# Performance work log

Hardware: AMD Instinct MI355X
Metric: run time of the kernel (lower is better)

## Reference

```python
import jax, jax.numpy as jnp
import numpy as np

N = 50000
EPS = 1e-16


def _gat_conv(x, w, att_src, att_dst, bias, src, dst, heads, out_ch, concat):
    # x: [N, F_in]; w: [heads*out_ch, F_in]; att_*: [heads, out_ch]; bias: [heads*out_ch] or [out_ch]
    n = x.shape[0]
    xw = (x @ w.T).reshape(n, heads, out_ch)              # [N, H, C]
    a_src = jnp.einsum('nhc,hc->nh', xw, att_src)          # [N, H]
    a_dst = jnp.einsum('nhc,hc->nh', xw, att_dst)
    alpha = a_src[src] + a_dst[dst]                        # [E, H]
    alpha = jax.nn.leaky_relu(alpha, negative_slope=0.2)
    # segment softmax over destination node (every node has a self loop)
    m = jax.ops.segment_max(alpha, dst, num_segments=n)    # [N, H]
    e = jnp.exp(alpha - m[dst])
    s = jax.ops.segment_sum(e, dst, num_segments=n)        # [N, H]
    coef = e / (s[dst] + EPS)                              # [E, H]
    out = jax.ops.segment_sum(xw[src] * coef[:, :, None], dst, num_segments=n)  # [N, H, C]
    if concat:
        out = out.reshape(n, heads * out_ch)
    else:
        out = out.mean(axis=1)
    return out + bias


def setup_inputs() -> dict:
    key = jax.random.key(0)
    ks = jax.random.split(key, 8)
    F_in, H, C1, NC = 128, 2, 64, 16
    E = 1_600_000
    x = jax.random.normal(ks[0], (N, F_in), dtype=jnp.float32)
    edge_index = jax.random.randint(ks[1], (2, E), 0, N, dtype=jnp.int64)
    w1 = jax.random.normal(ks[2], (H * C1, F_in), dtype=jnp.float32) / np.sqrt(F_in)
    att_src1 = jax.random.normal(ks[3], (H, C1), dtype=jnp.float32) / np.sqrt(C1)
    att_dst1 = jax.random.normal(ks[4], (H, C1), dtype=jnp.float32) / np.sqrt(C1)
    b1 = jnp.zeros((H * C1,), dtype=jnp.float32)
    w2 = jax.random.normal(ks[5], (NC, H * C1), dtype=jnp.float32) / np.sqrt(H * C1)
    att_src2 = jax.random.normal(ks[6], (1, NC), dtype=jnp.float32) / np.sqrt(NC)
    att_dst2 = jax.random.normal(ks[7], (1, NC), dtype=jnp.float32) / np.sqrt(NC)
    b2 = jnp.zeros((NC,), dtype=jnp.float32)
    return {"x": x, "edge_index": edge_index, "w1": w1, "att_src1": att_src1,
            "att_dst1": att_dst1, "b1": b1, "w2": w2, "att_src2": att_src2,
            "att_dst2": att_dst2, "b2": b2}


def reference(x, edge_index, w1, att_src1, att_dst1, b1, w2, att_src2, att_dst2, b2):
    n = x.shape[0]
    loop = jnp.arange(n, dtype=edge_index.dtype)
    src = jnp.concatenate([edge_index[0], loop])  # PyG adds self loops by default
    dst = jnp.concatenate([edge_index[1], loop])
    h = _gat_conv(x, w1, att_src1, att_dst1, b1, src, dst, heads=2, out_ch=64, concat=True)
    h = jax.nn.relu(h)
    # dropout p=0.5 is identity in eval mode
    out = _gat_conv(h, w2, att_src2, att_dst2, b2, src, dst, heads=1, out_ch=16, concat=True)
    return out
```

## Files before the change

### kernel.cpp

```cpp
#include <hip/hip_runtime.h>
#include <hip/hip_fp16.h>


#define BSHIFT 7
#define MAXB 512
#define CAPMAX 6144
#define XS 136

using f16x8 = __attribute__((ext_vector_type(8))) _Float16;
using f16x4 = __attribute__((ext_vector_type(4))) _Float16;
using f32x4 = __attribute__((ext_vector_type(4))) float;

__device__ __forceinline__ float lrelu(float a) { return fmaxf(a, 0.2f * a); }


__global__ __launch_bounds__(256) void part_gemm1_kernel(
    const int* __restrict__ src, const int* __restrict__ dst,
    int* __restrict__ bincur, unsigned* __restrict__ binned,
    int E, int B, int CH, int CAP, int NB,
    const float* __restrict__ x, const float* __restrict__ w1,
    const float* __restrict__ as1, const float* __restrict__ ad1,
    __half* __restrict__ xw1h, float* __restrict__ asrc1,
    float* __restrict__ adst1, int N) {
  __shared__ __align__(16) char smem[(64 + 128) * XS * 2];
  int t = threadIdx.x;

  if (blockIdx.x < (unsigned)NB) {
    int* s_h = (int*)smem;
    int* s_base = s_h + MAXB;
    int* s_cur = s_base + MAXB;
    unsigned* s_pack = (unsigned*)(s_cur + MAXB);
    for (int i = t; i < B; i += 256) s_h[i] = 0;
    __syncthreads();
    int lo = blockIdx.x * CH;
    int cnt = min(CH, E - lo);
    for (int i = t; i < cnt; i += 256) {
      int d = dst[lo + i];
      int s = src[lo + i];
      atomicAdd(&s_h[d >> BSHIFT], 1);
      s_pack[i] = (unsigned)s | ((unsigned)(d & 127) << 16) |
                  ((unsigned)(d >> BSHIFT) << 23);
    }
    __syncthreads();
    for (int i = t; i < B; i += 256) {
      int c = s_h[i];
      s_base[i] = c ? (i * CAP + atomicAdd(&bincur[i], c)) : 0;
      s_cur[i] = 0;
    }
    __syncthreads();
    for (int i = t; i < cnt; i += 256) {
      unsigned e = s_pack[i];
      int b = e >> 23;
      int r = atomicAdd(&s_cur[b], 1);
      binned[s_base[b] + r] = e & 0x7FFFFFu;
    }
    return;
  }

  _Float16* lx = (_Float16*)smem;
  _Float16* lw = lx + 64 * XS;
  int n0 = (blockIdx.x - NB) * 64;

#pragma unroll
  for (int j = 0; j < 8; ++j) {
    int idx = t + 256 * j;
    int nd = idx >> 5, i4 = (idx & 31) * 4;
    int gn = n0 + nd;
    float4 v = (gn < N) ? *(const float4*)&x[(size_t)gn * 128 + i4]
                        : make_float4(0.f, 0.f, 0.f, 0.f);
    f16x4 h;
    h[0] = (_Float16)v.x; h[1] = (_Float16)v.y;
    h[2] = (_Float16)v.z; h[3] = (_Float16)v.w;
    *(f16x4*)&lx[nd * XS + i4] = h;
  }
#pragma unroll
  for (int j = 0; j < 16; ++j) {
    int idx = t + 256 * j;
    int o = idx >> 5, i4 = (idx & 31) * 4;
    float4 v = *(const float4*)&w1[(size_t)o * 128 + i4];
    f16x4 h;
    h[0] = (_Float16)v.x; h[1] = (_Float16)v.y;
    h[2] = (_Float16)v.z; h[3] = (_Float16)v.w;
    *(f16x4*)&lw[o * XS + i4] = h;
  }
  __syncthreads();

  int lane = t & 63, wv = t >> 6;
  int m16 = lane & 15, q = lane >> 4;

  f32x4 acc[8];
#pragma unroll
  for (int i = 0; i < 8; ++i) acc[i] = (f32x4){0.f, 0.f, 0.f, 0.f};

#pragma unroll
  for (int c = 0; c < 4; ++c) {
    f16x8 a = *(const f16x8*)&lx[(16 * wv + m16) * XS + c * 32 + q * 8];
#pragma unroll
    for (int tt = 0; tt < 8; ++tt) {
      f16x8 b = *(const f16x8*)&lw[(tt * 16 + m16) * XS + c * 32 + q * 8];
      acc[tt] = __builtin_amdgcn_mfma_f32_16x16x32_f16(a, b, acc[tt], 0, 0, 0);
    }
  }

#pragma unroll
  for (int tt = 0; tt < 8; ++tt) {
#pragma unroll
    for (int r = 0; r < 4; ++r) {
      lx[(16 * wv + 4 * q + r) * XS + tt * 16 + m16] = (_Float16)acc[tt][r];
    }
  }

  {
    float ps = 0.f, pd = 0.f;
    int p = q;
#pragma unroll
    for (int k = 0; k < 4; ++k) {
      f16x8 hv = *(const f16x8*)&lx[(16 * wv + m16) * XS + p * 32 + k * 8];
      float4 s0 = *(const float4*)&as1[p * 32 + k * 8];
      float4 s1 = *(const float4*)&as1[p * 32 + k * 8 + 4];
      float4 d0 = *(const float4*)&ad1[p * 32 + k * 8];
      float4 d1 = *(const float4*)&ad1[p * 32 + k * 8 + 4];
      ps += (float)hv[0] * s0.x + (float)hv[1] * s0.y + (float)hv[2] * s0.z +
            (float)hv[3] * s0.w + (float)hv[4] * s1.x + (float)hv[5] * s1.y +
            (float)hv[6] * s1.z + (float)hv[7] * s1.w;
      pd += (float)hv[0] * d0.x + (float)hv[1] * d0.y + (float)hv[2] * d0.z +
            (float)hv[3] * d0.w + (float)hv[4] * d1.x + (float)hv[5] * d1.y +
            (float)hv[6] * d1.z + (float)hv[7] * d1.w;
    }
    ps += __shfl_xor(ps, 16);
    pd += __shfl_xor(pd, 16);
    int n = n0 + 16 * wv + m16;
    if (n < N && (q == 0 || q == 2)) {
      int hh = q >> 1;
      asrc1[2 * n + hh] = ps;
      adst1[2 * n + hh] = pd;
    }
  }

#pragma unroll
  for (int i = 0; i < 4; ++i) {
    int m = q + 4 * i;
    int n = n0 + 16 * wv + m;
    if (n < N) {
      uint4 v = *(const uint4*)&lx[(16 * wv + m) * XS + m16 * 8];
      *(uint4*)&xw1h[(size_t)n * 128 + m16 * 8] = v;
    }
  }
}


__global__ __launch_bounds__(256) void bucket_build_kernel(const unsigned* __restrict__ binned,
                                                           const int* __restrict__ bincur,
                                                           int2* __restrict__ nodeseg,
                                                           unsigned short* __restrict__ csr,
                                                           int N, int CAP) {
  __shared__ int s_deg[128];
  __shared__ int s_cur[128];
  __shared__ int s_wsum;
  __shared__ unsigned s_edges[CAPMAX];
  int b = blockIdx.x;
  int lo = b * CAP, hi = lo + bincur[b];
  int cnt = hi - lo;
  int t = threadIdx.x;
  if (t < 128) s_deg[t] = 0;
  int stg = min(cnt, CAPMAX);
  for (int i = t; i < stg; i += 256) s_edges[i] = binned[lo + i];
  __syncthreads();
  for (int i = t; i < cnt; i += 256) {
    unsigned e = (i < CAPMAX) ? s_edges[i] : binned[lo + i];
    atomicAdd(&s_deg[e >> 16], 1);
  }
  __syncthreads();
  int lane = t & 63, wv = t >> 6;
  int v = (t < 128) ? s_deg[t] : 0;
  int incl = v;
#pragma unroll
  for (int off = 1; off < 64; off <<= 1) {
    int u = __shfl_up(incl, off);
    if (lane >= off) incl += u;
  }
  if (t == 63) s_wsum = incl;
  __syncthreads();
  int excl = incl - v + ((wv == 1) ? s_wsum : 0);
  if (t < 128) {
    int node = (b << BSHIFT) + t;
    if (node < N) nodeseg[node] = make_int2(lo + excl, lo + excl + v);
    s_cur[t] = lo + excl;
  }
  __syncthreads();
  for (int i = t; i < cnt; i += 256) {
    unsigned e = (i < CAPMAX) ? s_edges[i] : binned[lo + i];
    int p = atomicAdd(&s_cur[e >> 16], 1);
    csr[p] = (unsigned short)(e & 0xFFFFu);
  }
}


__global__ __launch_bounds__(256) void agg1_kernel(const __half* __restrict__ xw1h,
                                                   const float* __restrict__ asrc1,
                                                   const float* __restrict__ adst1,
                                                   const float* __restrict__ b1,
                                                   const float* __restrict__ w2,
                                                   const float* __restrict__ as2,
                                                   const float* __restrict__ ad2,
                                                   const unsigned short* __restrict__ csr,
                                                   const int2* __restrict__ nodeseg,
                                                   __half* __restrict__ xw2h,
                                                   float* __restrict__ asrc2,
                                                   float* __restrict__ adst2, int N) {
  __shared__ int s_off[4][64];
  __shared__ float2 s_w[4][64];
  int lane = threadIdx.x & 63, wv = threadIdx.x >> 6;
  int d = blockIdx.x * 4 + wv;
  if (d >= N) return;
  int c8 = lane & 15;
  int row = lane >> 4;
  int head = c8 >> 3;
  int2 seg = nodeseg[d];
  int e0 = seg.x, e1 = seg.y;
  float2 asv = *(const float2*)&asrc1[2 * d];
  float2 adv = *(const float2*)&adst1[2 * d];
  float wself = __expf(lrelu(head ? (asv.y + adv.y) : (asv.x + adv.x)));

  const char* xb = (const char*)xw1h + 16 * c8;

  float a[8];
  float sum = 0.f;
#pragma unroll
  for (int k = 0; k < 8; ++k) a[k] = 0.f;
  if (row == 0) {
    uint4 r = *(const uint4*)(xb + ((size_t)d << 8));
    const __half2* hp = (const __half2*)&r;
#pragma unroll
    for (int k = 0; k < 4; ++k) {
      float2 v = __half22float2(hp[k]);
      a[2 * k] = wself * v.x;
      a[2 * k + 1] = wself * v.y;
    }
    sum = wself;
  }

  for (int base = e0; base < e1; base += 64) {
    int cnt = min(64, e1 - base);
    if (lane < cnt) {
      int s = (int)csr[base + lane];
      float2 aa = *(const float2*)&asrc1[2 * s];
      s_off[wv][lane] = s << 8;
      float2 w;
      w.x = __expf(lrelu(aa.x + adv.x));
      w.y = __expf(lrelu(aa.y + adv.y));
      s_w[wv][lane] = w;
    }
    int j = 0;
    for (; j + 7 < cnt; j += 8) {
      int oA = s_off[wv][j + row];
      int oB = s_off[wv][j + 4 + row];
      float wA = ((const float*)&s_w[wv][j + row])[head];
      float wB = ((const float*)&s_w[wv][j + 4 + row])[head];
      uint4 rA = *(const uint4*)(xb + oA);
      uint4 rB = *(const uint4*)(xb + oB);
      const __half2* hA = (const __half2*)&rA;
      const __half2* hB = (const __half2*)&rB;
#pragma unroll
      for (int k = 0; k < 4; ++k) {
        float2 vA = __half22float2(hA[k]);
        float2 vB = __half22float2(hB[k]);
        a[2 * k] += wA * vA.x + wB * vB.x;
        a[2 * k + 1] += wA * vA.y + wB * vB.y;
      }
      sum += wA + wB;
    }
    for (; j < cnt; j += 4) {
      if (row < cnt - j) {
        int oA = s_off[wv][j + row];
        float wA = ((const float*)&s_w[wv][j + row])[head];
        uint4 rA = *(const uint4*)(xb + oA);
        const __half2* hA = (const __half2*)&rA;
#pragma unroll
        for (int k = 0; k < 4; ++k) {
          float2 vA = __half22float2(hA[k]);
          a[2 * k] += wA * vA.x;
          a[2 * k + 1] += wA * vA.y;
        }
        sum += wA;
      }
    }
  }

#pragma unroll
  for (int k = 0; k < 8; ++k) {
    a[k] += __shfl_xor(a[k], 16);
    a[k] += __shfl_xor(a[k], 32);
  }
  sum += __shfl_xor(sum, 16);
  sum += __shfl_xor(sum, 32);

  float inv = 1.f / (sum + 1e-16f);
  float4 blo = *(const float4*)&b1[8 * c8];
  float4 bhi = *(const float4*)&b1[8 * c8 + 4];
  float h[8];
  h[0] = fmaxf(a[0] * inv + blo.x, 0.f);
  h[1] = fmaxf(a[1] * inv + blo.y, 0.f);
  h[2] = fmaxf(a[2] * inv + blo.z, 0.f);
  h[3] = fmaxf(a[3] * inv + blo.w, 0.f);
  h[4] = fmaxf(a[4] * inv + bhi.x, 0.f);
  h[5] = fmaxf(a[5] * inv + bhi.y, 0.f);
  h[6] = fmaxf(a[6] * inv + bhi.z, 0.f);
  h[7] = fmaxf(a[7] * inv + bhi.w, 0.f);

  float p[4];
#pragma unroll
  for (int cc = 0; cc < 4; ++cc) {
    const float4 wlo = *(const float4*)&w2[(row * 4 + cc) * 128 + 8 * c8];
    const float4 whi = *(const float4*)&w2[(row * 4 + cc) * 128 + 8 * c8 + 4];
    p[cc] = h[0] * wlo.x + h[1] * wlo.y + h[2] * wlo.z + h[3] * wlo.w +
            h[4] * whi.x + h[5] * whi.y + h[6] * whi.z + h[7] * whi.w;
#pragma unroll
    for (int k = 1; k < 16; k <<= 1) p[cc] += __shfl_xor(p[cc], k);
  }
  float qs = 0.f, qd = 0.f;
#pragma unroll
  for (int cc = 0; cc < 4; ++cc) {
    qs += p[cc] * as2[row * 4 + cc];
    qd += p[cc] * ad2[row * 4 + cc];
  }
  qs += __shfl_xor(qs, 16);
  qs += __shfl_xor(qs, 32);
  qd += __shfl_xor(qd, 16);
  qd += __shfl_xor(qd, 32);
  if (lane == 0) {
    asrc2[d] = qs;
    adst2[d] = qd;
  }
  if (c8 == 0) {
    union {
      __half hh[4];
      uint2 u;
    } pk;
#pragma unroll
    for (int cc = 0; cc < 4; ++cc) pk.hh[cc] = __float2half(p[cc]);
    *(uint2*)&xw2h[(size_t)d * 16 + row * 4] = pk.u;
  }
}


__global__ __launch_bounds__(256) void agg2_kernel(const __half* __restrict__ xw2h,
                                                   const float* __restrict__ asrc2,
                                                   const float* __restrict__ adst2,
                                                   const float* __restrict__ b2,
                                                   const unsigned short* __restrict__ csr,
                                                   const int2* __restrict__ nodeseg,
                                                   float* __restrict__ out, int N) {
  __shared__ int s_off[4][64];
  __shared__ float s_w[4][64];
  int lane = threadIdx.x & 63, wv = threadIdx.x >> 6;
  int d = blockIdx.x * 4 + wv;
  if (d >= N) return;
  int c2 = lane & 7;
  int row = lane >> 3;
  int2 seg = nodeseg[d];
  int e0 = seg.x, e1 = seg.y;
  float advd = adst2[d];
  float wself = __expf(lrelu(asrc2[d] + advd));
  const char* xb = (const char*)xw2h + 4 * c2;

  float a0 = 0.f, a1 = 0.f, sum = 0.f;
  if (row == 0) {
    float2 v = __half22float2(*(const __half2*)(xb + (size_t)d * 32));
    a0 = wself * v.x;
    a1 = wself * v.y;
    sum = wself;
  }
  for (int base = e0; base < e1; base += 64) {
    int cnt = min(64, e1 - base);
    if (lane < cnt) {
      int s = (int)csr[base + lane];
      s_off[wv][lane] = s << 5;
      s_w[wv][lane] = __expf(lrelu(asrc2[s] + advd));
    }
    int j = 0;
    for (; j + 15 < cnt; j += 16) {
      int o0 = s_off[wv][j + row];
      int o1 = s_off[wv][j + 8 + row];
      float w0 = s_w[wv][j + row];
      float w1 = s_w[wv][j + 8 + row];
      float2 v0 = __half22float2(*(const __half2*)(xb + o0));
      float2 v1 = __half22float2(*(const __half2*)(xb + o1));
      a0 += w0 * v0.x + w1 * v1.x;
      a1 += w0 * v0.y + w1 * v1.y;
      sum += w0 + w1;
    }
    for (; j + 7 < cnt; j += 8) {
      int o0 = s_off[wv][j + row];
      float w0 = s_w[wv][j + row];
      float2 v0 = __half22float2(*(const __half2*)(xb + o0));
      a0 += w0 * v0.x;
      a1 += w0 * v0.y;
      sum += w0;
    }
    if (row < cnt - j) {
      int o0 = s_off[wv][j + row];
      float w0 = s_w[wv][j + row];
      float2 v0 = __half22float2(*(const __half2*)(xb + o0));
      a0 += w0 * v0.x;
      a1 += w0 * v0.y;
      sum += w0;
    }
  }
#pragma unroll
  for (int k = 8; k < 64; k <<= 1) {
    a0 += __shfl_xor(a0, k);
    a1 += __shfl_xor(a1, k);
    sum += __shfl_xor(sum, k);
  }
  if (lane < 8) {
    float inv = 1.f / (sum + 1e-16f);
    float2 r;
    r.x = a0 * inv + b2[2 * c2];
    r.y = a1 * inv + b2[2 * c2 + 1];
    *(float2*)&out[(size_t)d * 16 + 2 * c2] = r;
  }
}


extern "C" void kernel_launch(void* const* d_in, const int* in_sizes, int n_in,
                              void* d_out, int out_size, void* d_ws, size_t ws_size,
                              hipStream_t stream) {
  const float* x = (const float*)d_in[0];
  const int* ei = (const int*)d_in[1];
  const float* w1 = (const float*)d_in[2];
  const float* as1 = (const float*)d_in[3];
  const float* ad1 = (const float*)d_in[4];
  const float* b1 = (const float*)d_in[5];
  const float* w2 = (const float*)d_in[6];
  const float* as2 = (const float*)d_in[7];
  const float* ad2 = (const float*)d_in[8];
  const float* b2 = (const float*)d_in[9];
  float* out = (float*)d_out;

  int N = in_sizes[0] / 128;
  int E = in_sizes[1] / 2;
  const int* srcp = ei;
  const int* dstp = ei + E;

  int B = (N + (1 << BSHIFT) - 1) >> BSHIFT;
  int mean = (E + B - 1) / B;
  int CAP = (mean + mean / 4 + 512 + 255) & ~255;
  const int NB = 256;
  int CH = (E + NB - 1) / NB;
  int GB = (N + 63) / 64;

  char* p = (char*)d_ws;
  auto alloc = [&](size_t bytes) -> void* {
    void* r = (void*)p;
    p += (bytes + 255) & ~(size_t)255;
    return r;
  };
  __half* xw1h = (__half*)alloc((size_t)N * 128 * 2);
  float* asrc1 = (float*)alloc((size_t)N * 2 * 4);
  float* adst1 = (float*)alloc((size_t)N * 2 * 4);
  __half* xw2h = (__half*)alloc((size_t)N * 16 * 2);
  float* asrc2 = (float*)alloc((size_t)N * 4);
  float* adst2 = (float*)alloc((size_t)N * 4);
  int2* nodeseg = (int2*)alloc((size_t)N * 8);
  unsigned short* csr = (unsigned short*)alloc((size_t)B * CAP * 2);
  unsigned* binned = (unsigned*)alloc((size_t)B * CAP * 4);
  int* bincur = (int*)alloc((size_t)B * 4);

  hipMemsetAsync(bincur, 0, (size_t)B * 4, stream);
  part_gemm1_kernel<<<NB + GB, 256, 0, stream>>>(srcp, dstp, bincur, binned,
                                                 E, B, CH, CAP, NB,
                                                 x, w1, as1, ad1, xw1h, asrc1, adst1, N);
  bucket_build_kernel<<<B, 256, 0, stream>>>(binned, bincur, nodeseg, csr, N, CAP);
  agg1_kernel<<<(N + 3) / 4, 256, 0, stream>>>(xw1h, asrc1, adst1, b1, w2, as2, ad2,
                                               csr, nodeseg, xw2h, asrc2, adst2, N);
  agg2_kernel<<<(N + 3) / 4, 256, 0, stream>>>(xw2h, asrc2, adst2, b2, csr, nodeseg, out, N);
}
```

Before: 210.2 us.

## Split layer-1 aggregation per head and add a combine kernel for layer-2 projection

The layer-1 aggregation kernel now runs one wavefront per (node, head) instead of per node. Each head's 64 channels are covered by 8 lanes, and 8 edges are processed per step, unrolled to 16. Each head writes its partial layer-2 projection to a new fp32 buffer. A new combine kernel sums the two head partials, writes the fp16 xw2 and computes the layer-2 attention logits. The aim is more parallelism and more edges in flight per gather step, at the cost of reading the CSR and edge weights twice, extra global traffic for the partial buffer, and one more kernel launch.

```diff
diff --git a/kernel.cpp b/kernel.cpp
--- a/kernel.cpp
+++ b/kernel.cpp
@@ -196,33 +196,28 @@
 }
 
 
-__global__ __launch_bounds__(256) void agg1_kernel(const __half* __restrict__ xw1h,
-                                                   const float* __restrict__ asrc1,
-                                                   const float* __restrict__ adst1,
-                                                   const float* __restrict__ b1,
-                                                   const float* __restrict__ w2,
-                                                   const float* __restrict__ as2,
-                                                   const float* __restrict__ ad2,
-                                                   const unsigned short* __restrict__ csr,
-                                                   const int2* __restrict__ nodeseg,
-                                                   __half* __restrict__ xw2h,
-                                                   float* __restrict__ asrc2,
-                                                   float* __restrict__ adst2, int N) {
+__global__ __launch_bounds__(256) void agg1h_kernel(const __half* __restrict__ xw1h,
+                                                    const float* __restrict__ asrc1,
+                                                    const float* __restrict__ adst1,
+                                                    const float* __restrict__ b1,
+                                                    const float* __restrict__ w2,
+                                                    const unsigned short* __restrict__ csr,
+                                                    const int2* __restrict__ nodeseg,
+                                                    float* __restrict__ p_out, int N) {
   __shared__ int s_off[4][64];
-  __shared__ float2 s_w[4][64];
+  __shared__ float s_w[4][64];
   int lane = threadIdx.x & 63, wv = threadIdx.x >> 6;
-  int d = blockIdx.x * 4 + wv;
+  int head = blockIdx.x & 1;
+  int d = (blockIdx.x >> 1) * 4 + wv;
   if (d >= N) return;
-  int c8 = lane & 15;
-  int row = lane >> 4;
-  int head = c8 >> 3;
+  int c8 = lane & 7;
+  int row = lane >> 3;
   int2 seg = nodeseg[d];
   int e0 = seg.x, e1 = seg.y;
-  float2 asv = *(const float2*)&asrc1[2 * d];
-  float2 adv = *(const float2*)&adst1[2 * d];
-  float wself = __expf(lrelu(head ? (asv.y + adv.y) : (asv.x + adv.x)));
-
-  const char* xb = (const char*)xw1h + 16 * c8;
+  float adv = adst1[2 * d + head];
+  float wself = __expf(lrelu(asrc1[2 * d + head] + adv));
+
+  const char* xb = (const char*)xw1h + (head << 7) + 16 * c8;
 
   float a[8];
   float sum = 0.f;
@@ -244,19 +239,15 @@
     int cnt = min(64, e1 - base);
     if (lane < cnt) {
       int s = (int)csr[base + lane];
-      float2 aa = *(const float2*)&asrc1[2 * s];
       s_off[wv][lane] = s << 8;
-      float2 w;
-      w.x = __expf(lrelu(aa.x + adv.x));
-      w.y = __expf(lrelu(aa.y + adv.y));
-      s_w[wv][lane] = w;
+      s_w[wv][lane] = __expf(lrelu(asrc1[2 * s + head] + adv));
     }
     int j = 0;
-    for (; j + 7 < cnt; j += 8) {
+    for (; j + 15 < cnt; j += 16) {
       int oA = s_off[wv][j + row];
-      int oB = s_off[wv][j + 4 + row];
-      float wA = ((const float*)&s_w[wv][j + row])[head];
-      float wB = ((const float*)&s_w[wv][j + 4 + row])[head];
+      int oB = s_off[wv][j + 8 + row];
+      float wA = s_w[wv][j + row];
+      float wB = s_w[wv][j + 8 + row];
       uint4 rA = *(const uint4*)(xb + oA);
       uint4 rB = *(const uint4*)(xb + oB);
       const __half2* hA = (const __half2*)&rA;
@@ -270,34 +261,48 @@
       }
       sum += wA + wB;
     }
-    for (; j < cnt; j += 4) {
-      if (row < cnt - j) {
-        int oA = s_off[wv][j + row];
-        float wA = ((const float*)&s_w[wv][j + row])[head];
-        uint4 rA = *(const uint4*)(xb + oA);
-        const __half2* hA = (const __half2*)&rA;
-#pragma unroll
-        for (int k = 0; k < 4; ++k) {
-          float2 vA = __half22float2(hA[k]);
-          a[2 * k] += wA * vA.x;
-          a[2 * k + 1] += wA * vA.y;
-        }
-        sum += wA;
+    for (; j + 7 < cnt; j += 8) {
+      int oA = s_off[wv][j + row];
+      float wA = s_w[wv][j + row];
+      uint4 rA = *(const uint4*)(xb + oA);
+      const __half2* hA = (const __half2*)&rA;
+#pragma unroll
+      for (int k = 0; k < 4; ++k) {
+        float2 vA = __half22float2(hA[k]);
+        a[2 * k] += wA * vA.x;
+        a[2 * k + 1] += wA * vA.y;
       }
+      sum += wA;
+    }
+    if (row < cnt - j) {
+      int oA = s_off[wv][j + row];
+      float wA = s_w[wv][j + row];
+      uint4 rA = *(const uint4*)(xb + oA);
+      const __half2* hA = (const __half2*)&rA;
+#pragma unroll
+      for (int k = 0; k < 4; ++k) {
+        float2 vA = __half22float2(hA[k]);
+        a[2 * k] += wA * vA.x;
+        a[2 * k + 1] += wA * vA.y;
+      }
+      sum += wA;
     }
   }
 
 #pragma unroll
   for (int k = 0; k < 8; ++k) {
+    a[k] += __shfl_xor(a[k], 8);
     a[k] += __shfl_xor(a[k], 16);
     a[k] += __shfl_xor(a[k], 32);
   }
+  sum += __shfl_xor(sum, 8);
   sum += __shfl_xor(sum, 16);
   sum += __shfl_xor(sum, 32);
 
   float inv = 1.f / (sum + 1e-16f);
-  float4 blo = *(const float4*)&b1[8 * c8];
-  float4 bhi = *(const float4*)&b1[8 * c8 + 4];
+  int cb = head * 64 + 8 * c8;
+  float4 blo = *(const float4*)&b1[cb];
+  float4 bhi = *(const float4*)&b1[cb + 4];
   float h[8];
   h[0] = fmaxf(a[0] * inv + blo.x, 0.f);
   h[1] = fmaxf(a[1] * inv + blo.y, 0.f);
@@ -308,38 +313,51 @@
   h[6] = fmaxf(a[6] * inv + bhi.z, 0.f);
   h[7] = fmaxf(a[7] * inv + bhi.w, 0.f);
 
-  float p[4];
-#pragma unroll
-  for (int cc = 0; cc < 4; ++cc) {
-    const float4 wlo = *(const float4*)&w2[(row * 4 + cc) * 128 + 8 * c8];
-    const float4 whi = *(const float4*)&w2[(row * 4 + cc) * 128 + 8 * c8 + 4];
-    p[cc] = h[0] * wlo.x + h[1] * wlo.y + h[2] * wlo.z + h[3] * wlo.w +
-            h[4] * whi.x + h[5] * whi.y + h[6] * whi.z + h[7] * whi.w;
-#pragma unroll
-    for (int k = 1; k < 16; k <<= 1) p[cc] += __shfl_xor(p[cc], k);
-  }
-  float qs = 0.f, qd = 0.f;
-#pragma unroll
-  for (int cc = 0; cc < 4; ++cc) {
-    qs += p[cc] * as2[row * 4 + cc];
-    qd += p[cc] * ad2[row * 4 + cc];
-  }
-  qs += __shfl_xor(qs, 16);
-  qs += __shfl_xor(qs, 32);
-  qd += __shfl_xor(qd, 16);
-  qd += __shfl_xor(qd, 32);
-  if (lane == 0) {
-    asrc2[d] = qs;
-    adst2[d] = qd;
+  float p0, p1;
+  {
+    const float* wr0 = &w2[(size_t)(2 * row) * 128 + cb];
+    const float* wr1 = &w2[(size_t)(2 * row + 1) * 128 + cb];
+    float4 w0lo = *(const float4*)wr0;
+    float4 w0hi = *(const float4*)(wr0 + 4);
+    float4 w1lo = *(const float4*)wr1;
+    float4 w1hi = *(const float4*)(wr1 + 4);
+    p0 = h[0] * w0lo.x + h[1] * w0lo.y + h[2] * w0lo.z + h[3] * w0lo.w +
+         h[4] * w0hi.x + h[5] * w0hi.y + h[6] * w0hi.z + h[7] * w0hi.w;
+    p1 = h[0] * w1lo.x + h[1] * w1lo.y + h[2] * w1lo.z + h[3] * w1lo.w +
+         h[4] * w1hi.x + h[5] * w1hi.y + h[6] * w1hi.z + h[7] * w1hi.w;
+  }
+#pragma unroll
+  for (int k = 1; k < 8; k <<= 1) {
+    p0 += __shfl_xor(p0, k);
+    p1 += __shfl_xor(p1, k);
   }
   if (c8 == 0) {
-    union {
-      __half hh[4];
-      uint2 u;
-    } pk;
-#pragma unroll
-    for (int cc = 0; cc < 4; ++cc) pk.hh[cc] = __float2half(p[cc]);
-    *(uint2*)&xw2h[(size_t)d * 16 + row * 4] = pk.u;
+    *(float2*)&p_out[(size_t)d * 32 + head * 16 + 2 * row] =
+        make_float2(p0, p1);
+  }
+}
+
+
+__global__ __launch_bounds__(256) void combine_kernel(const float* __restrict__ p,
+                                                      const float* __restrict__ as2,
+                                                      const float* __restrict__ ad2,
+                                                      __half* __restrict__ xw2h,
+                                                      float* __restrict__ asrc2,
+                                                      float* __restrict__ adst2, int N) {
+  int idx = blockIdx.x * 256 + threadIdx.x;
+  int node = idx >> 4, c = idx & 15;
+  if (node >= N) return;
+  float v = p[(size_t)node * 32 + c] + p[(size_t)node * 32 + 16 + c];
+  xw2h[(size_t)node * 16 + c] = __float2half(v);
+  float qs = v * as2[c], qd = v * ad2[c];
+#pragma unroll
+  for (int k = 1; k < 16; k <<= 1) {
+    qs += __shfl_xor(qs, k);
+    qd += __shfl_xor(qd, k);
+  }
+  if (c == 0) {
+    asrc2[node] = qs;
+    adst2[node] = qd;
   }
 }
 
@@ -462,6 +480,7 @@
   __half* xw2h = (__half*)alloc((size_t)N * 16 * 2);
   float* asrc2 = (float*)alloc((size_t)N * 4);
   float* adst2 = (float*)alloc((size_t)N * 4);
+  float* p_out = (float*)alloc((size_t)N * 32 * 4);
   int2* nodeseg = (int2*)alloc((size_t)N * 8);
   unsigned short* csr = (unsigned short*)alloc((size_t)B * CAP * 2);
   unsigned* binned = (unsigned*)alloc((size_t)B * CAP * 4);
@@ -472,7 +491,9 @@
                                                  E, B, CH, CAP, NB,
                                                  x, w1, as1, ad1, xw1h, asrc1, adst1, N);
   bucket_build_kernel<<<B, 256, 0, stream>>>(binned, bincur, nodeseg, csr, N, CAP);
-  agg1_kernel<<<(N + 3) / 4, 256, 0, stream>>>(xw1h, asrc1, adst1, b1, w2, as2, ad2,
-                                               csr, nodeseg, xw2h, asrc2, adst2, N);
+  agg1h_kernel<<<2 * ((N + 3) / 4), 256, 0, stream>>>(xw1h, asrc1, adst1, b1, w2,
+                                                      csr, nodeseg, p_out, N);
+  combine_kernel<<<(N * 16 + 255) / 256, 256, 0, stream>>>(p_out, as2, ad2,
+                                                           xw2h, asrc2, adst2, N);
   agg2_kernel<<<(N + 3) / 4, 256, 0, stream>>>(xw2h, asrc2, adst2, b2, csr, nodeseg, out, N);
 }
```

After: 215.6 us. 2.5% more time.

## Locally sort edges in shared memory to coalesce binned and CSR writes

Applied to the files above, without the earlier changes.

The partition blocks now prefix-scan their per-bucket histogram and counting-sort their edge chunk in shared memory. Edges are then written to the global binned array in bucket-contiguous runs instead of scattered atomic-ordered stores. The bucket build kernel likewise assembles the CSR segment in shared memory and copies it out linearly. The partition block count also rises from 256 to 320 so the doubled shared-memory staging fits. The cost is extra LDS traffic, one more barrier pass and a wave-serial scan per block.

```diff
diff --git a/kernel.cpp b/kernel.cpp
--- a/kernel.cpp
+++ b/kernel.cpp
@@ -6,6 +6,7 @@
 #define MAXB 512
 #define CAPMAX 6144
 #define XS 136
+#define NBP 320
 
 using f16x8 = __attribute__((ext_vector_type(8))) _Float16;
 using f16x4 = __attribute__((ext_vector_type(4))) _Float16;
@@ -17,7 +18,7 @@
 __global__ __launch_bounds__(256) void part_gemm1_kernel(
     const int* __restrict__ src, const int* __restrict__ dst,
     int* __restrict__ bincur, unsigned* __restrict__ binned,
-    int E, int B, int CH, int CAP, int NB,
+    int E, int B, int CH, int CAP,
     const float* __restrict__ x, const float* __restrict__ w1,
     const float* __restrict__ as1, const float* __restrict__ ad1,
     __half* __restrict__ xw1h, float* __restrict__ asrc1,
@@ -25,12 +26,15 @@
   __shared__ __align__(16) char smem[(64 + 128) * XS * 2];
   int t = threadIdx.x;
 
-  if (blockIdx.x < (unsigned)NB) {
+  if (blockIdx.x < (unsigned)NBP) {
     int* s_h = (int*)smem;
     int* s_base = s_h + MAXB;
     int* s_cur = s_base + MAXB;
-    unsigned* s_pack = (unsigned*)(s_cur + MAXB);
-    for (int i = t; i < B; i += 256) s_h[i] = 0;
+    int* s_lbase = s_cur + MAXB;
+    unsigned* s_pack = (unsigned*)(s_lbase + MAXB);
+    unsigned* s_sorted = s_pack + CH;
+    int lane = t & 63, wv = t >> 6;
+    for (int i = t; i < MAXB; i += 256) s_h[i] = 0;
     __syncthreads();
     int lo = blockIdx.x * CH;
     int cnt = min(CH, E - lo);
@@ -42,24 +46,46 @@
                   ((unsigned)(d >> BSHIFT) << 23);
     }
     __syncthreads();
+    if (wv == 0) {
+      int run = 0;
+#pragma unroll
+      for (int c = 0; c < MAXB / 64; ++c) {
+        int idx = c * 64 + lane;
+        int v = s_h[idx];
+        int incl = v;
+#pragma unroll
+        for (int off = 1; off < 64; off <<= 1) {
+          int u = __shfl_up(incl, off);
+          if (lane >= off) incl += u;
+        }
+        s_lbase[idx] = run + incl - v;
+        run += __shfl(incl, 63);
+      }
+    }
+    __syncthreads();
     for (int i = t; i < B; i += 256) {
       int c = s_h[i];
       s_base[i] = c ? (i * CAP + atomicAdd(&bincur[i], c)) : 0;
-      s_cur[i] = 0;
+      s_cur[i] = s_lbase[i];
     }
     __syncthreads();
     for (int i = t; i < cnt; i += 256) {
       unsigned e = s_pack[i];
+      int r = atomicAdd(&s_cur[e >> 23], 1);
+      s_sorted[r] = e;
+    }
+    __syncthreads();
+    for (int j = t; j < cnt; j += 256) {
+      unsigned e = s_sorted[j];
       int b = e >> 23;
-      int r = atomicAdd(&s_cur[b], 1);
-      binned[s_base[b] + r] = e & 0x7FFFFFu;
+      binned[s_base[b] + (j - s_lbase[b])] = e & 0x7FFFFFu;
     }
     return;
   }
 
   _Float16* lx = (_Float16*)smem;
   _Float16* lw = lx + 64 * XS;
-  int n0 = (blockIdx.x - NB) * 64;
+  int n0 = (blockIdx.x - NBP) * 64;
 
 #pragma unroll
   for (int j = 0; j < 8; ++j) {
@@ -158,6 +184,7 @@
   __shared__ int s_cur[128];
   __shared__ int s_wsum;
   __shared__ unsigned s_edges[CAPMAX];
+  __shared__ unsigned short s_csr[CAPMAX];
   int b = blockIdx.x;
   int lo = b * CAP, hi = lo + bincur[b];
   int cnt = hi - lo;
@@ -185,14 +212,16 @@
   if (t < 128) {
     int node = (b << BSHIFT) + t;
     if (node < N) nodeseg[node] = make_int2(lo + excl, lo + excl + v);
-    s_cur[t] = lo + excl;
+    s_cur[t] = excl;
   }
   __syncthreads();
   for (int i = t; i < cnt; i += 256) {
     unsigned e = (i < CAPMAX) ? s_edges[i] : binned[lo + i];
     int p = atomicAdd(&s_cur[e >> 16], 1);
-    csr[p] = (unsigned short)(e & 0xFFFFu);
-  }
+    s_csr[p] = (unsigned short)(e & 0xFFFFu);
+  }
+  __syncthreads();
+  for (int j = t; j < cnt; j += 256) csr[lo + j] = s_csr[j];
 }
 
 
@@ -446,8 +475,7 @@
   int B = (N + (1 << BSHIFT) - 1) >> BSHIFT;
   int mean = (E + B - 1) / B;
   int CAP = (mean + mean / 4 + 512 + 255) & ~255;
-  const int NB = 256;
-  int CH = (E + NB - 1) / NB;
+  int CH = (E + NBP - 1) / NBP;
   int GB = (N + 63) / 64;
 
   char* p = (char*)d_ws;
@@ -468,9 +496,9 @@
   int* bincur = (int*)alloc((size_t)B * 4);
 
   hipMemsetAsync(bincur, 0, (size_t)B * 4, stream);
-  part_gemm1_kernel<<<NB + GB, 256, 0, stream>>>(srcp, dstp, bincur, binned,
-                                                 E, B, CH, CAP, NB,
-                                                 x, w1, as1, ad1, xw1h, asrc1, adst1, N);
+  part_gemm1_kernel<<<NBP + GB, 256, 0, stream>>>(srcp, dstp, bincur, binned,
+                                                  E, B, CH, CAP,
+                                                  x, w1, as1, ad1, xw1h, asrc1, adst1, N);
   bucket_build_kernel<<<B, 256, 0, stream>>>(binned, bincur, nodeseg, csr, N, CAP);
   agg1_kernel<<<(N + 3) / 4, 256, 0, stream>>>(xw1h, asrc1, adst1, b1, w2, as2, ad2,
                                                csr, nodeseg, xw2h, asrc2, adst2, N);
```

Result: no change. 206.3 us (-1.9%).
